# Kernel optimization log

Hardware: AMD Instinct MI355X
Metric: run time of the kernel (lower is better)

Reference implementation:

```python
import jax, jax.numpy as jnp
import numpy as np

B, T, H, M, S, E, IN = 8, 2048, 64, 32, 20, 3, 32
EPS = 1e-8  # torch CosineSimilarity eps


def setup_inputs() -> dict:
    key = jax.random.key(0)
    ks = jax.random.split(key, 7)
    return {
        "x": jax.random.normal(ks[0], (B, T, IN), jnp.float32),
        "hidden": jax.random.normal(ks[1], (E, B, T, H), jnp.float32),
        "memory": jax.random.normal(ks[2], (S, M), jnp.float32),
        "Wq": jax.random.normal(ks[3], (E, H, M), jnp.float32),
        "Wk": jax.random.normal(ks[4], (E, H, M), jnp.float32),
        "Wv": jax.random.normal(ks[5], (E, H, M), jnp.float32),
        "input_query": jax.random.normal(ks[6], (IN, M), jnp.float32),
    }


def _cosine(a, b):
    # torch.nn.CosineSimilarity(dim=-1): each vector norm clamped to eps
    na = jnp.maximum(jnp.linalg.norm(a, axis=-1), EPS)
    nb = jnp.maximum(jnp.linalg.norm(b, axis=-1), EPS)
    return jnp.sum(a * b, axis=-1) / (na * nb)


def reference(x, hidden, memory, Wq, Wk, Wv, input_query):
    # query_mem: soft read from global memory slots
    q_in = jnp.einsum('bti,im->btm', x, input_query)           # [B,T,M]
    mem_sc = jax.nn.softmax(jnp.einsum('btm,sm->bts', q_in, memory), axis=-1)
    memories = jnp.einsum('bts,sm->btm', mem_sc, memory)       # [B,T,M]

    # per-expert tiny self-attention (vectorized over expert axis e)
    Q = jnp.einsum('ebth,ehm->ebtm', hidden, Wq)
    K = jnp.einsum('ebth,ehm->ebtm', hidden, Wk)
    V = jnp.einsum('ebth,ehm->ebtm', hidden, Wv)
    energy = jnp.einsum('ebtm,ebsm->ebts', Q, K)               # [E,B,T,T]
    att = jax.nn.softmax(energy, axis=-1)
    out = jnp.einsum('ebts,ebsm->ebtm', att, V)                # [E,B,T,M]

    cos = _cosine(memories[None], out)                         # [E,B,T]
    return jnp.moveaxis(cos, 0, -1)                            # [B,T,E]
```

## Files before the change

kernel.cpp:

```cpp
#include <hip/hip_runtime.h>
#include <hip/hip_bf16.h>

#define Bv  8
#define Tv  2048
#define Hv  64
#define Mv  32
#define Sv  20
#define Ev  3
#define INv 32
#define LOG2E 1.44269504088896340736f

typedef __attribute__((ext_vector_type(8))) _Float16 half8;
typedef __attribute__((ext_vector_type(2))) __fp16 fp16x2;
typedef __attribute__((ext_vector_type(4))) float float4v;

__global__ __launch_bounds__(256) void mem_kernel(
    const float* __restrict__ x,
    const float* __restrict__ memory,
    const float* __restrict__ iq,
    float* __restrict__ memout)
{
    __shared__ float sIQ[32][32];
    __shared__ float sM[20][32];
    int tid = threadIdx.x;
    for (int i = tid; i < 32 * 32; i += 256) sIQ[i >> 5][i & 31] = iq[i];
    for (int i = tid; i < 20 * 32; i += 256) sM[i >> 5][i & 31] = memory[i];
    __syncthreads();

    int t = blockIdx.x * 256 + tid;
    const float4* xr = (const float4*)(x + (size_t)t * INv);
    float xv[32];
#pragma unroll
    for (int i = 0; i < 8; ++i) {
        float4 v = xr[i];
        xv[4*i] = v.x; xv[4*i+1] = v.y; xv[4*i+2] = v.z; xv[4*i+3] = v.w;
    }
    float qm[32];
#pragma unroll
    for (int m = 0; m < 32; ++m) qm[m] = 0.f;
    for (int i = 0; i < 32; ++i) {
        float xi = xv[i];
#pragma unroll
        for (int m4 = 0; m4 < 8; ++m4) {
            float4 wv = *(const float4*)&sIQ[i][m4 * 4];
            qm[4*m4]   = fmaf(xi, wv.x, qm[4*m4]);
            qm[4*m4+1] = fmaf(xi, wv.y, qm[4*m4+1]);
            qm[4*m4+2] = fmaf(xi, wv.z, qm[4*m4+2]);
            qm[4*m4+3] = fmaf(xi, wv.w, qm[4*m4+3]);
        }
    }
    float sc[20];
#pragma unroll
    for (int j = 0; j < 20; ++j) {
        float acc = 0.f;
#pragma unroll
        for (int m = 0; m < 32; ++m) acc = fmaf(qm[m], sM[j][m], acc);
        sc[j] = acc;
    }
    float mx = sc[0];
#pragma unroll
    for (int j = 1; j < 20; ++j) mx = fmaxf(mx, sc[j]);
    float psum = 0.f, p[20];
#pragma unroll
    for (int j = 0; j < 20; ++j) { p[j] = exp2f((sc[j] - mx) * LOG2E); psum += p[j]; }
    float inv = 1.0f / psum;
    float mo[32];
#pragma unroll
    for (int m = 0; m < 32; ++m) mo[m] = 0.f;
    for (int j = 0; j < 20; ++j) {
        float pj = p[j];
#pragma unroll
        for (int m = 0; m < 32; ++m) mo[m] = fmaf(pj, sM[j][m], mo[m]);
    }
    float4* outp = (float4*)(memout + (size_t)t * Mv);
#pragma unroll
    for (int m4 = 0; m4 < 8; ++m4) {
        float4 v;
        v.x = mo[4*m4] * inv; v.y = mo[4*m4+1] * inv;
        v.z = mo[4*m4+2] * inv; v.w = mo[4*m4+3] * inv;
        outp[m4] = v;
    }
}

__global__ __launch_bounds__(256) void qkv_kernel(
    const float* __restrict__ hidden,
    const float* __restrict__ Wq,
    const float* __restrict__ Wk,
    const float* __restrict__ Wv,
    _Float16* __restrict__ Qh, _Float16* __restrict__ Ql,
    _Float16* __restrict__ Kh, _Float16* __restrict__ Kl,
    _Float16* __restrict__ Vth)
{
    __shared__ __align__(16) char qsm[43008];
    float* sHT = (float*)qsm;
    float* sW  = (float*)(qsm + 17408);

    int bid  = blockIdx.x;
    int tile = bid & 31;
    int b    = (bid >> 5) & 7;
    int e    = bid >> 8;
    int tid  = threadIdx.x;
    size_t eb = (size_t)(e * Bv + b);
    size_t row0 = eb * Tv + (size_t)tile * 64;
    const float* hbase = hidden + row0 * Hv;

    {
        int r  = tid >> 2;
        int c4 = tid & 3;
#pragma unroll
        for (int hh = 0; hh < 4; ++hh) {
            int h4 = c4 + hh * 4;
            float4 v = ((const float4*)(hbase + (size_t)r * Hv))[h4];
            sHT[(h4*4+0)*68 + r] = v.x; sHT[(h4*4+1)*68 + r] = v.y;
            sHT[(h4*4+2)*68 + r] = v.z; sHT[(h4*4+3)*68 + r] = v.w;
        }
    }
    {
        const float* wq = Wq + (size_t)e * Hv * Mv;
        const float* wk = Wk + (size_t)e * Hv * Mv;
        const float* wv = Wv + (size_t)e * Hv * Mv;
        for (int i = tid; i < Hv * Mv; i += 256) {
            int h = i >> 5, m = i & 31;
            sW[h*100 + m]      = wq[i];
            sW[h*100 + 32 + m] = wk[i];
            sW[h*100 + 64 + m] = wv[i];
        }
    }
    __syncthreads();

    int ty = tid >> 4, tx = tid & 15;
    float acc[4][6];
#pragma unroll
    for (int i = 0; i < 4; ++i)
#pragma unroll
        for (int j = 0; j < 6; ++j) acc[i][j] = 0.f;

    for (int h = 0; h < 64; ++h) {
        float4 av = *(const float4*)&sHT[h*68 + ty * 4];
        float a[4] = {av.x, av.y, av.z, av.w};
        float bb[6];
#pragma unroll
        for (int j = 0; j < 6; ++j) bb[j] = sW[h*100 + tx * 6 + j];
#pragma unroll
        for (int i = 0; i < 4; ++i)
#pragma unroll
            for (int j = 0; j < 6; ++j) acc[i][j] = fmaf(a[i], bb[j], acc[i][j]);
    }

    __syncthreads();
    char* sQh = qsm;
    char* sQl = qsm + 4096;
    char* sKh = qsm + 8192;
    char* sKl = qsm + 12288;
    char* sVh = qsm + 16384;
#pragma unroll
    for (int i = 0; i < 4; ++i) {
        int row = ty * 4 + i;
#pragma unroll
        for (int j = 0; j < 6; ++j) {
            int c = tx * 6 + j;
            float v = acc[i][j];
            if (c < 32) {
                v *= LOG2E;
                _Float16 h16 = (_Float16)v;
                _Float16 l16 = (_Float16)(v - (float)h16);
                *(_Float16*)(sQh + row * 64 + c * 2) = h16;
                *(_Float16*)(sQl + row * 64 + c * 2) = l16;
            } else if (c < 64) {
                _Float16 h16 = (_Float16)v;
                _Float16 l16 = (_Float16)(v - (float)h16);
                int m = c - 32, q = m >> 3, wi = m & 7;
                int off = row * 64 + (((q + row) & 3) << 4) + wi * 2;
                *(_Float16*)(sKh + off) = h16;
                *(_Float16*)(sKl + off) = l16;
            } else {
                int d = c - 64, c8 = row >> 3, wi = row & 7;
                int off = d * 128 + (((c8 + d) & 7) << 4) + wi * 2;
                *(_Float16*)(sVh + off) = (_Float16)v;
            }
        }
    }
    __syncthreads();

    size_t pb = eb * (size_t)Tv * 32 + (size_t)tile * 2048;
    _Float16* dsts[5] = {Qh + pb, Ql + pb, Kh + pb, Kl + pb, Vth + pb};
#pragma unroll
    for (int pl = 0; pl < 5; ++pl)
        ((float4*)dsts[pl])[tid] = ((const float4*)(qsm + pl * 4096))[tid];
}

__device__ __forceinline__ void load_lds16(const _Float16* g, char* l) {
    __builtin_amdgcn_global_load_lds(
        (const __attribute__((address_space(1))) void*)g,
        (__attribute__((address_space(3))) void*)l, 16, 0, 0);
}

__global__ __launch_bounds__(256, 1) void attn_kernel(
    const _Float16* __restrict__ Qh, const _Float16* __restrict__ Ql,
    const _Float16* __restrict__ Kh, const _Float16* __restrict__ Kl,
    const _Float16* __restrict__ Vth,
    const float* __restrict__ memv,
    float* __restrict__ out)
{
    __shared__ __align__(16) char smem[32768];
    const int PW = 24576;

    int bid  = blockIdx.x;
    int xcd  = bid & 7;
    int slot = bid >> 3;
    int tile = slot & 31;
    int ebi  = xcd + ((slot >> 5) << 3);
    int e    = ebi >> 3;
    int b    = ebi & 7;
    int tid  = threadIdx.x;
    int lane = tid & 63;
    int w    = tid >> 6;
    int quad = lane >> 4;
    int l15  = lane & 15;
    size_t eb = (size_t)ebi;
    int q0 = tile * 64 + w * 16;

    size_t qoff = (eb * Tv + (size_t)(q0 + l15)) * 32 + quad * 8;
    half8 qH = *(const half8*)(Qh + qoff);
    half8 qL = *(const half8*)(Ql + qoff);

    float4v O0 = {0.f, 0.f, 0.f, 0.f};
    float4v O1 = {0.f, 0.f, 0.f, 0.f};
    float m_run = -3.0e38f;

    size_t ebOff = eb * (size_t)Tv * 32;
    const _Float16* gp[3] = {Kh + ebOff, Kl + ebOff, Vth + ebOff};

#pragma unroll
    for (int j = 0; j < 3; ++j) {
        int idx = w * 3 + j, p = idx >> 2, k = idx & 3;
        load_lds16(gp[p] + (size_t)k * 512 + lane * 8,
                   smem + p * 4096 + k * 1024);
    }

    for (int c = 0; c < 32; ++c) {
        int pb = c & 1;
        __syncthreads();
        if (c + 1 < 32) {
#pragma unroll
            for (int j = 0; j < 3; ++j) {
                int idx = w * 3 + j, p = idx >> 2, k = idx & 3;
                load_lds16(gp[p] + (size_t)(c + 1) * 2048 + k * 512 + lane * 8,
                           smem + (pb ^ 1) * 12288 + p * 4096 + k * 1024);
            }
        }
        const char* base = smem + pb * 12288;

        float s[16];
        float cmax = -3.0e38f;
#pragma unroll
        for (int tau = 0; tau < 4; ++tau) {
            int r = tau * 16 + l15;
            int sw = ((quad + r) & 3) << 4;
            half8 aH = *(const half8*)(base + r * 64 + sw);
            half8 aL = *(const half8*)(base + 4096 + r * 64 + sw);
            float4v acc = {0.f, 0.f, 0.f, 0.f};
            acc = __builtin_amdgcn_mfma_f32_16x16x32_f16(aH, qL, acc, 0, 0, 0);
            acc = __builtin_amdgcn_mfma_f32_16x16x32_f16(aL, qH, acc, 0, 0, 0);
            acc = __builtin_amdgcn_mfma_f32_16x16x32_f16(aH, qH, acc, 0, 0, 0);
#pragma unroll
            for (int r2 = 0; r2 < 4; ++r2) {
                s[tau * 4 + r2] = acc[r2];
                cmax = fmaxf(cmax, acc[r2]);
            }
        }
        cmax = fmaxf(cmax, __shfl_xor(cmax, 16));
        cmax = fmaxf(cmax, __shfl_xor(cmax, 32));
        float mNew  = fmaxf(m_run, cmax);
        float alpha = exp2f(m_run - mNew);
#pragma unroll
        for (int i = 0; i < 16; ++i)
            s[i] = exp2f(s[i] - mNew);
        m_run = mNew;

#pragma unroll
        for (int r = 0; r < 4; ++r) {
            float ar = __shfl(alpha, quad * 4 + r, 16);
            O0[r] *= ar;
            O1[r] *= ar;
        }

        char* pw = smem + PW + w * 2048 + l15 * 128;
        int xr = l15 & 7;
#pragma unroll
        for (int tau = 0; tau < 4; ++tau) {
            fp16x2 h01 = __builtin_amdgcn_cvt_pkrtz(s[tau*4+0], s[tau*4+1]);
            fp16x2 h23 = __builtin_amdgcn_cvt_pkrtz(s[tau*4+2], s[tau*4+3]);
            uint2 u;
            u.x = __builtin_bit_cast(unsigned int, h01);
            u.y = __builtin_bit_cast(unsigned int, h23);
            int bi = tau * 2 + (quad >> 1);
            *(uint2*)(pw + ((bi ^ xr) << 4) + (quad & 1) * 8) = u;
        }
        __asm__ volatile("" ::: "memory");

#pragma unroll
        for (int ks = 0; ks < 2; ++ks) {
            int swv = ((ks * 4 + quad + l15) & 7) << 4;
            half8 pA  = *(const half8*)(pw + (((ks * 4 + quad) ^ xr) << 4));
            half8 v0H = *(const half8*)(base + 8192 + l15 * 128 + swv);
            half8 v1H = *(const half8*)(base + 8192 + (16 + l15) * 128 + swv);
            O0 = __builtin_amdgcn_mfma_f32_16x16x32_f16(pA, v0H, O0, 0, 0, 0);
            O1 = __builtin_amdgcn_mfma_f32_16x16x32_f16(pA, v1H, O1, 0, 0, 0);
        }
    }

    const float* mb = memv + (size_t)b * Tv * 32;
    float dotr[4], nor[4], nmr[4];
#pragma unroll
    for (int r = 0; r < 4; ++r) {
        int trow = q0 + quad * 4 + r;
        float mv0 = mb[(size_t)trow * 32 + l15];
        float mv1 = mb[(size_t)trow * 32 + 16 + l15];
        float d  = O0[r] * mv0 + O1[r] * mv1;
        float n  = O0[r] * O0[r] + O1[r] * O1[r];
        float nm = mv0 * mv0 + mv1 * mv1;
#pragma unroll
        for (int delta = 1; delta < 16; delta <<= 1) {
            d  += __shfl_xor(d,  delta);
            n  += __shfl_xor(n,  delta);
            nm += __shfl_xor(nm, delta);
        }
        dotr[r] = d; nor[r] = n; nmr[r] = nm;
    }
    if (l15 < 4) {
        int r = l15;
        float na = fmaxf(sqrtf(nmr[r]), 1e-8f);
        float nb = fmaxf(sqrtf(nor[r]), 1e-30f);
        float cosv = dotr[r] / (na * nb);
        int trow = q0 + quad * 4 + r;
        out[((size_t)b * Tv + trow) * Ev + e] = cosv;
    }
}

extern "C" void kernel_launch(void* const* d_in, const int* in_sizes, int n_in,
                              void* d_out, int out_size, void* d_ws, size_t ws_size,
                              hipStream_t stream) {
    const float* x      = (const float*)d_in[0];
    const float* hidden = (const float*)d_in[1];
    const float* memory = (const float*)d_in[2];
    const float* Wq     = (const float*)d_in[3];
    const float* Wk     = (const float*)d_in[4];
    const float* Wv     = (const float*)d_in[5];
    const float* iq     = (const float*)d_in[6];
    float* out          = (float*)d_out;

    char* ws = (char*)d_ws;
    const size_t PLANE = (size_t)Ev * Bv * Tv * 32 * 2;
    float*    memout = (float*)ws;
    _Float16* Qh  = (_Float16*)(ws + 2097152);
    _Float16* Ql  = (_Float16*)(ws + 2097152 + PLANE);
    _Float16* Kh  = (_Float16*)(ws + 2097152 + 2 * PLANE);
    _Float16* Kl  = (_Float16*)(ws + 2097152 + 3 * PLANE);
    _Float16* Vth = (_Float16*)(ws + 2097152 + 4 * PLANE);

    mem_kernel<<<(Bv * Tv) / 256, 256, 0, stream>>>(x, memory, iq, memout);
    qkv_kernel<<<Ev * Bv * (Tv / 64), 256, 0, stream>>>(hidden, Wq, Wk, Wv,
                                                        Qh, Ql, Kh, Kl, Vth);
    attn_kernel<<<Ev * Bv * (Tv / 64), 256, 0, stream>>>(Qh, Ql, Kh, Kl, Vth,
                                                         memout, out);
}
```

Before: 157.7 us.

## Fuse memory-read into QKV kernel, retune LDS swizzles, skip redundant rescale

```diff
diff --git a/kernel.cpp b/kernel.cpp
--- a/kernel.cpp
+++ b/kernel.cpp
@@ -14,84 +14,22 @@
 typedef __attribute__((ext_vector_type(2))) __fp16 fp16x2;
 typedef __attribute__((ext_vector_type(4))) float float4v;
 
-__global__ __launch_bounds__(256) void mem_kernel(
-    const float* __restrict__ x,
-    const float* __restrict__ memory,
-    const float* __restrict__ iq,
-    float* __restrict__ memout)
-{
-    __shared__ float sIQ[32][32];
-    __shared__ float sM[20][32];
-    int tid = threadIdx.x;
-    for (int i = tid; i < 32 * 32; i += 256) sIQ[i >> 5][i & 31] = iq[i];
-    for (int i = tid; i < 20 * 32; i += 256) sM[i >> 5][i & 31] = memory[i];
-    __syncthreads();
-
-    int t = blockIdx.x * 256 + tid;
-    const float4* xr = (const float4*)(x + (size_t)t * INv);
-    float xv[32];
-#pragma unroll
-    for (int i = 0; i < 8; ++i) {
-        float4 v = xr[i];
-        xv[4*i] = v.x; xv[4*i+1] = v.y; xv[4*i+2] = v.z; xv[4*i+3] = v.w;
-    }
-    float qm[32];
-#pragma unroll
-    for (int m = 0; m < 32; ++m) qm[m] = 0.f;
-    for (int i = 0; i < 32; ++i) {
-        float xi = xv[i];
-#pragma unroll
-        for (int m4 = 0; m4 < 8; ++m4) {
-            float4 wv = *(const float4*)&sIQ[i][m4 * 4];
-            qm[4*m4]   = fmaf(xi, wv.x, qm[4*m4]);
-            qm[4*m4+1] = fmaf(xi, wv.y, qm[4*m4+1]);
-            qm[4*m4+2] = fmaf(xi, wv.z, qm[4*m4+2]);
-            qm[4*m4+3] = fmaf(xi, wv.w, qm[4*m4+3]);
-        }
-    }
-    float sc[20];
-#pragma unroll
-    for (int j = 0; j < 20; ++j) {
-        float acc = 0.f;
-#pragma unroll
-        for (int m = 0; m < 32; ++m) acc = fmaf(qm[m], sM[j][m], acc);
-        sc[j] = acc;
-    }
-    float mx = sc[0];
-#pragma unroll
-    for (int j = 1; j < 20; ++j) mx = fmaxf(mx, sc[j]);
-    float psum = 0.f, p[20];
-#pragma unroll
-    for (int j = 0; j < 20; ++j) { p[j] = exp2f((sc[j] - mx) * LOG2E); psum += p[j]; }
-    float inv = 1.0f / psum;
-    float mo[32];
-#pragma unroll
-    for (int m = 0; m < 32; ++m) mo[m] = 0.f;
-    for (int j = 0; j < 20; ++j) {
-        float pj = p[j];
-#pragma unroll
-        for (int m = 0; m < 32; ++m) mo[m] = fmaf(pj, sM[j][m], mo[m]);
-    }
-    float4* outp = (float4*)(memout + (size_t)t * Mv);
-#pragma unroll
-    for (int m4 = 0; m4 < 8; ++m4) {
-        float4 v;
-        v.x = mo[4*m4] * inv; v.y = mo[4*m4+1] * inv;
-        v.z = mo[4*m4+2] * inv; v.w = mo[4*m4+3] * inv;
-        outp[m4] = v;
-    }
-}
-
 __global__ __launch_bounds__(256) void qkv_kernel(
     const float* __restrict__ hidden,
     const float* __restrict__ Wq,
     const float* __restrict__ Wk,
     const float* __restrict__ Wv,
+    const float* __restrict__ x,
+    const float* __restrict__ memory,
+    const float* __restrict__ iq,
     _Float16* __restrict__ Qh, _Float16* __restrict__ Ql,
     _Float16* __restrict__ Kh, _Float16* __restrict__ Kl,
-    _Float16* __restrict__ Vth)
+    _Float16* __restrict__ Vth,
+    float* __restrict__ memout)
 {
     __shared__ __align__(16) char qsm[43008];
+    __shared__ float sIQ[32][32];
+    __shared__ float sM[20][32];
     float* sHT = (float*)qsm;
     float* sW  = (float*)(qsm + 17408);
 
@@ -103,6 +41,9 @@
     size_t eb = (size_t)(e * Bv + b);
     size_t row0 = eb * Tv + (size_t)tile * 64;
     const float* hbase = hidden + row0 * Hv;
+
+    for (int i = tid; i < 32 * 32; i += 256) sIQ[i >> 5][i & 31] = iq[i];
+    for (int i = tid; i < 20 * 32; i += 256) sM[i >> 5][i & 31] = memory[i];
 
     {
         int r  = tid >> 2;
@@ -170,7 +111,7 @@
                 _Float16 h16 = (_Float16)v;
                 _Float16 l16 = (_Float16)(v - (float)h16);
                 int m = c - 32, q = m >> 3, wi = m & 7;
-                int off = row * 64 + (((q + row) & 3) << 4) + wi * 2;
+                int off = row * 64 + (((q + row + (row >> 2)) & 3) << 4) + wi * 2;
                 *(_Float16*)(sKh + off) = h16;
                 *(_Float16*)(sKl + off) = l16;
             } else {
@@ -187,6 +128,62 @@
 #pragma unroll
     for (int pl = 0; pl < 5; ++pl)
         ((float4*)dsts[pl])[tid] = ((const float4*)(qsm + pl * 4096))[tid];
+
+    if (e == 0 && tid < 64) {
+        int t = b * Tv + tile * 64 + tid;
+        const float4* xr = (const float4*)(x + (size_t)t * INv);
+        float xv[32];
+#pragma unroll
+        for (int i = 0; i < 8; ++i) {
+            float4 v = xr[i];
+            xv[4*i] = v.x; xv[4*i+1] = v.y; xv[4*i+2] = v.z; xv[4*i+3] = v.w;
+        }
+        float qm[32];
+#pragma unroll
+        for (int m = 0; m < 32; ++m) qm[m] = 0.f;
+        for (int i = 0; i < 32; ++i) {
+            float xi = xv[i];
+#pragma unroll
+            for (int m4 = 0; m4 < 8; ++m4) {
+                float4 wv = *(const float4*)&sIQ[i][m4 * 4];
+                qm[4*m4]   = fmaf(xi, wv.x, qm[4*m4]);
+                qm[4*m4+1] = fmaf(xi, wv.y, qm[4*m4+1]);
+                qm[4*m4+2] = fmaf(xi, wv.z, qm[4*m4+2]);
+                qm[4*m4+3] = fmaf(xi, wv.w, qm[4*m4+3]);
+            }
+        }
+        float sc[20];
+#pragma unroll
+        for (int j = 0; j < 20; ++j) {
+            float a2 = 0.f;
+#pragma unroll
+            for (int m = 0; m < 32; ++m) a2 = fmaf(qm[m], sM[j][m], a2);
+            sc[j] = a2;
+        }
+        float mx = sc[0];
+#pragma unroll
+        for (int j = 1; j < 20; ++j) mx = fmaxf(mx, sc[j]);
+        float psum = 0.f, p[20];
+#pragma unroll
+        for (int j = 0; j < 20; ++j) { p[j] = exp2f((sc[j] - mx) * LOG2E); psum += p[j]; }
+        float inv = 1.0f / psum;
+        float mo[32];
+#pragma unroll
+        for (int m = 0; m < 32; ++m) mo[m] = 0.f;
+        for (int j = 0; j < 20; ++j) {
+            float pj = p[j];
+#pragma unroll
+            for (int m = 0; m < 32; ++m) mo[m] = fmaf(pj, sM[j][m], mo[m]);
+        }
+        float4* outp = (float4*)(memout + (size_t)t * Mv);
+#pragma unroll
+        for (int m4 = 0; m4 < 8; ++m4) {
+            float4 v;
+            v.x = mo[4*m4] * inv; v.y = mo[4*m4+1] * inv;
+            v.z = mo[4*m4+2] * inv; v.w = mo[4*m4+3] * inv;
+            outp[m4] = v;
+        }
+    }
 }
 
 __device__ __forceinline__ void load_lds16(const _Float16* g, char* l) {
@@ -202,7 +199,7 @@
     const float* __restrict__ memv,
     float* __restrict__ out)
 {
-    __shared__ __align__(16) char smem[32768];
+    __shared__ __align__(16) char smem[33280];
     const int PW = 24576;
 
     int bid  = blockIdx.x;
@@ -239,24 +236,24 @@
     }
 
     for (int c = 0; c < 32; ++c) {
-        int pb = c & 1;
+        int pbuf = c & 1;
         __syncthreads();
         if (c + 1 < 32) {
 #pragma unroll
             for (int j = 0; j < 3; ++j) {
                 int idx = w * 3 + j, p = idx >> 2, k = idx & 3;
                 load_lds16(gp[p] + (size_t)(c + 1) * 2048 + k * 512 + lane * 8,
-                           smem + (pb ^ 1) * 12288 + p * 4096 + k * 1024);
-            }
-        }
-        const char* base = smem + pb * 12288;
+                           smem + (pbuf ^ 1) * 12288 + p * 4096 + k * 1024);
+            }
+        }
+        const char* base = smem + pbuf * 12288;
 
         float s[16];
         float cmax = -3.0e38f;
 #pragma unroll
         for (int tau = 0; tau < 4; ++tau) {
             int r = tau * 16 + l15;
-            int sw = ((quad + r) & 3) << 4;
+            int sw = ((quad + r + (r >> 2)) & 3) << 4;
             half8 aH = *(const half8*)(base + r * 64 + sw);
             half8 aL = *(const half8*)(base + 4096 + r * 64 + sw);
             float4v acc = {0.f, 0.f, 0.f, 0.f};
@@ -271,22 +268,24 @@
         }
         cmax = fmaxf(cmax, __shfl_xor(cmax, 16));
         cmax = fmaxf(cmax, __shfl_xor(cmax, 32));
-        float mNew  = fmaxf(m_run, cmax);
-        float alpha = exp2f(m_run - mNew);
+        float mNew = fmaxf(m_run, cmax);
+
+        if (__ballot(mNew > m_run)) {
+            float alpha = exp2f(m_run - mNew);
+#pragma unroll
+            for (int r = 0; r < 4; ++r) {
+                float ar = __shfl(alpha, quad * 4 + r, 16);
+                O0[r] *= ar;
+                O1[r] *= ar;
+            }
+        }
+        m_run = mNew;
+
 #pragma unroll
         for (int i = 0; i < 16; ++i)
             s[i] = exp2f(s[i] - mNew);
-        m_run = mNew;
-
-#pragma unroll
-        for (int r = 0; r < 4; ++r) {
-            float ar = __shfl(alpha, quad * 4 + r, 16);
-            O0[r] *= ar;
-            O1[r] *= ar;
-        }
-
-        char* pw = smem + PW + w * 2048 + l15 * 128;
-        int xr = l15 & 7;
+
+        char* pw = smem + PW + w * 2176 + l15 * 136;
 #pragma unroll
         for (int tau = 0; tau < 4; ++tau) {
             fp16x2 h01 = __builtin_amdgcn_cvt_pkrtz(s[tau*4+0], s[tau*4+1]);
@@ -294,15 +293,14 @@
             uint2 u;
             u.x = __builtin_bit_cast(unsigned int, h01);
             u.y = __builtin_bit_cast(unsigned int, h23);
-            int bi = tau * 2 + (quad >> 1);
-            *(uint2*)(pw + ((bi ^ xr) << 4) + (quad & 1) * 8) = u;
+            *(uint2*)(pw + tau * 32 + quad * 8) = u;
         }
         __asm__ volatile("" ::: "memory");
 
 #pragma unroll
         for (int ks = 0; ks < 2; ++ks) {
             int swv = ((ks * 4 + quad + l15) & 7) << 4;
-            half8 pA  = *(const half8*)(pw + (((ks * 4 + quad) ^ xr) << 4));
+            half8 pA  = *(const half8*)(pw + ks * 64 + quad * 16);
             half8 v0H = *(const half8*)(base + 8192 + l15 * 128 + swv);
             half8 v1H = *(const half8*)(base + 8192 + (16 + l15) * 128 + swv);
             O0 = __builtin_amdgcn_mfma_f32_16x16x32_f16(pA, v0H, O0, 0, 0, 0);
@@ -359,9 +357,9 @@
     _Float16* Kl  = (_Float16*)(ws + 2097152 + 3 * PLANE);
     _Float16* Vth = (_Float16*)(ws + 2097152 + 4 * PLANE);
 
-    mem_kernel<<<(Bv * Tv) / 256, 256, 0, stream>>>(x, memory, iq, memout);
     qkv_kernel<<<Ev * Bv * (Tv / 64), 256, 0, stream>>>(hidden, Wq, Wk, Wv,
-                                                        Qh, Ql, Kh, Kl, Vth);
+                                                        x, memory, iq,
+                                                        Qh, Ql, Kh, Kl, Vth, memout);
     attn_kernel<<<Ev * Bv * (Tv / 64), 256, 0, stream>>>(Qh, Ql, Kh, Kl, Vth,
                                                          memout, out);
 }
```

After: 159.3 us. Within noise of the previous version (+1.0%).
